# Kernel tuning notes

Hardware: AMD Instinct MI355X
Metric: run time of the kernel (lower is better)

The kernel has to match this reference:

```python
import jax, jax.numpy as jnp
import numpy as np

B, T, I, H, L, O = 32, 2048, 256, 512, 2, 256


def _cell(xg, h, c, Whh, bhh):
    # xg: precomputed/current input-to-hidden projection incl. b_ih, shape [B, 4H]
    gates = xg + h @ Whh.T + bhh
    i, f, g, o = jnp.split(gates, 4, axis=-1)
    i = jax.nn.sigmoid(i)
    f = jax.nn.sigmoid(f)
    g = jnp.tanh(g)
    o = jax.nn.sigmoid(o)
    c2 = f * c + i * g
    h2 = o * jnp.tanh(c2)
    return h2, c2


def setup_inputs() -> dict:
    key = jax.random.key(0)
    ks = jax.random.split(key, 11)
    s_i = 1.0 / np.sqrt(H)
    return {
        "x": jax.random.normal(ks[0], (B, T, I), jnp.float32),
        "W_ih0": jax.random.normal(ks[1], (4 * H, I), jnp.float32) * s_i,
        "W_hh0": jax.random.normal(ks[2], (4 * H, H), jnp.float32) * s_i,
        "b_ih0": jax.random.normal(ks[3], (4 * H,), jnp.float32) * s_i,
        "b_hh0": jax.random.normal(ks[4], (4 * H,), jnp.float32) * s_i,
        "W_ih1": jax.random.normal(ks[5], (4 * H, H), jnp.float32) * s_i,
        "W_hh1": jax.random.normal(ks[6], (4 * H, H), jnp.float32) * s_i,
        "b_ih1": jax.random.normal(ks[7], (4 * H,), jnp.float32) * s_i,
        "b_hh1": jax.random.normal(ks[8], (4 * H,), jnp.float32) * s_i,
        "fc_w": jax.random.normal(ks[9], (O, H), jnp.float32) * s_i,
        "fc_b": jax.random.normal(ks[10], (O,), jnp.float32) * s_i,
    }


def reference(x, W_ih0, W_hh0, b_ih0, b_hh0, W_ih1, W_hh1, b_ih1, b_hh1, fc_w, fc_b):
    # Precompute layer-0 input projections for all timesteps in one big GEMM.
    xproj = jnp.einsum('bti,gi->tbg', x, W_ih0) + b_ih0  # [T, B, 4H]

    h0 = jnp.zeros((x.shape[0], H), x.dtype)
    carry0 = (h0, h0, h0, h0)  # (h_l0, c_l0, h_l1, c_l1)

    def step(carry, xg_t):
        h_0, c_0, h_1, c_1 = carry
        h_0, c_0 = _cell(xg_t, h_0, c_0, W_hh0, b_hh0)
        xg1 = h_0 @ W_ih1.T + b_ih1
        h_1, c_1 = _cell(xg1, h_1, c_1, W_hh1, b_hh1)
        return (h_0, c_0, h_1, c_1), None

    (h_0, c_0, h_1, c_1), _ = jax.lax.scan(step, carry0, xproj)
    # Original takes last timestep's top-layer hidden, then fc.
    return h_1 @ fc_w.T + fc_b
```

## Files before the change

kernel.cpp:

```cpp
#include <hip/hip_runtime.h>
#include <hip/hip_bf16.h>

typedef __hip_bfloat16 bf16;
typedef unsigned long long u64;
typedef unsigned int u32;
typedef unsigned short u16;
using short8 = __attribute__((ext_vector_type(8))) short;
using f32x4  = __attribute__((ext_vector_type(4))) float;

#define T_STEPS 2048
#define IDIM    256
#define HDIM    512
#define NBLK    128
#define R0      8
#define HWW     8192
#define LROW    528
#define TAGMASK 0x0000ffff0000ffffULL

__device__ __forceinline__ float sigm(float x) { return 1.0f / (1.0f + __expf(-x)); }
__device__ __forceinline__ float tanh_f(float x) {
  x = fminf(fmaxf(x, -15.f), 15.f);
  float e = __expf(2.f * x);
  return (e - 1.f) / (e + 1.f);
}
__device__ __forceinline__ u16 bfbits(float f) {
  bf16 b = __float2bfloat16(f); u16 s; __builtin_memcpy(&s, &b, 2); return s;
}
__device__ __forceinline__ short8 cvt8(const float* __restrict__ p) {
  float4 lo = *(const float4*)(const void*)p;
  float4 hi = *(const float4*)(const void*)(p + 4);
  short8 r;
  r[0] = (short)bfbits(lo.x); r[1] = (short)bfbits(lo.y); r[2] = (short)bfbits(lo.z); r[3] = (short)bfbits(lo.w);
  r[4] = (short)bfbits(hi.x); r[5] = (short)bfbits(hi.y); r[6] = (short)bfbits(hi.z); r[7] = (short)bfbits(hi.w);
  return r;
}

__device__ __forceinline__ u64 ldg8(const u64* p) {
  return __hip_atomic_load(p, __ATOMIC_RELAXED, __HIP_MEMORY_SCOPE_AGENT);
}
__device__ __forceinline__ u32 ldg4(const u32* p) {
  return __hip_atomic_load(p, __ATOMIC_RELAXED, __HIP_MEMORY_SCOPE_AGENT);
}
__device__ __forceinline__ void stg4(u32* p, u32 v) {
  __hip_atomic_store(p, v, __ATOMIC_RELAXED, __HIP_MEMORY_SCOPE_AGENT);
}

__device__ __forceinline__ int wave_min_i(int v) {
#pragma unroll
  for (int off = 32; off > 0; off >>= 1) {
    int o = __shfl_xor(v, off, 64);
    v = v < o ? v : o;
  }
  return v;
}

__device__ __forceinline__ void ldsw(bf16* dst, int i, int tid, u64 v) {
  u32 lo = (u32)v, hi = (u32)(v >> 32);
  *(u32*)(void*)(dst + i * LROW + tid * 2) = (lo >> 16) | (hi & 0xffff0000u);
}

__device__ __forceinline__ void pollstage(const u32* __restrict__ src, bf16* dst,
                                          int tid, u32 tag) {
  const u64* s = (const u64*)(const void*)src;
  const u64 tt = ((u64)tag << 32) | tag;
  u64 v[16];
#pragma unroll
  for (int i = 0; i < 16; i++) v[i] = ldg8(s + tid + i * 256);
  unsigned bad = 0xffffu;
  while (bad) {
    unsigned nb = 0;
#pragma unroll
    for (int i = 0; i < 16; i++)
      if (bad & (1u << i)) {
        if ((v[i] & TAGMASK) != tt) { v[i] = ldg8(s + tid + i * 256); nb |= 1u << i; }
      }
    bad = nb;
  }
#pragma unroll
  for (int i = 0; i < 16; i++) ldsw(dst, i, tid, v[i]);
}

__device__ __forceinline__ void poll2stage(const u32* __restrict__ s0p, bf16* d0, u32 tag0,
                                           const u32* __restrict__ s1p, bf16* d1, u32 tag1,
                                           int tid) {
  const u64* s0 = (const u64*)(const void*)s0p;
  const u64* s1 = (const u64*)(const void*)s1p;
  const u64 tt0 = ((u64)tag0 << 32) | tag0;
  const u64 tt1 = ((u64)tag1 << 32) | tag1;
  u64 v0[16], v1[16];
#pragma unroll
  for (int i = 0; i < 16; i++) v0[i] = ldg8(s0 + tid + i * 256);
#pragma unroll
  for (int i = 0; i < 16; i++) v1[i] = ldg8(s1 + tid + i * 256);
  unsigned bad0 = 0xffffu, bad1 = 0xffffu;
  while (bad0 | bad1) {
    unsigned nb0 = 0, nb1 = 0;
#pragma unroll
    for (int i = 0; i < 16; i++)
      if (bad0 & (1u << i)) {
        if ((v0[i] & TAGMASK) != tt0) { v0[i] = ldg8(s0 + tid + i * 256); nb0 |= 1u << i; }
      }
#pragma unroll
    for (int i = 0; i < 16; i++)
      if (bad1 & (1u << i)) {
        if ((v1[i] & TAGMASK) != tt1) { v1[i] = ldg8(s1 + tid + i * 256); nb1 |= 1u << i; }
      }
    bad0 = nb0; bad1 = nb1;
  }
#pragma unroll
  for (int i = 0; i < 16; i++) ldsw(d0, i, tid, v0[i]);
#pragma unroll
  for (int i = 0; i < 16; i++) ldsw(d1, i, tid, v1[i]);
}

#define MFMA(a, b, c) __builtin_amdgcn_mfma_f32_16x16x32_bf16((a), (b), (c), 0, 0, 0)

__global__ void __launch_bounds__(256, 1) lstm_tagged2p(
    const float* __restrict__ x,
    const float* __restrict__ Wih0, const float* __restrict__ Whh0,
    const float* __restrict__ bih0, const float* __restrict__ bhh0,
    const float* __restrict__ Wih1, const float* __restrict__ Whh1,
    const float* __restrict__ bih1, const float* __restrict__ bhh1,
    const float* __restrict__ fcw, const float* __restrict__ fcb,
    float* __restrict__ out,
    u32* __restrict__ ring0g,
    u32* __restrict__ ring1g) {
  __shared__ __align__(16) bf16 lds_h0[16 * LROW];
  __shared__ __align__(16) bf16 lds_h1[16 * LROW];

  const int tid  = threadIdx.x;
  const int w    = tid >> 6, lane = tid & 63;
  const int q    = lane >> 4, m = lane & 15, q8 = q * 8;
  const int bx   = (int)blockIdx.x;
  const int g    = bx >> 6;
  const int rr   = bx & 63;
  const bool l0  = (rr < 32);
  const int blk  = rr & 31;
  const int jb   = blk * 16 + w * 4;
  const int unit = jb + (m >> 2), gate = m & 3;
  const int wrow = gate * HDIM + unit;
  const int ju   = jb + q;
  const f32x4 zero = {0.f, 0.f, 0.f, 0.f};

  u32* ring0 = ring0g + (size_t)g * R0 * HWW;
  u32* ring1 = ring1g + (size_t)g * 2 * HWW;

  short8 A[32];
  f32x4 bias;
  if (l0) {
#pragma unroll
    for (int kc = 0; kc < 8; kc++)  A[kc]      = cvt8(Wih0 + wrow * IDIM + kc * 32 + q8);
#pragma unroll
    for (int kc = 0; kc < 16; kc++) A[8 + kc]  = cvt8(Whh0 + wrow * HDIM + kc * 32 + q8);
#pragma unroll
    for (int r = 0; r < 4; r++)
      bias[r] = bih0[r * HDIM + ju] + bhh0[r * HDIM + ju];
  } else {
#pragma unroll
    for (int kc = 0; kc < 16; kc++) A[kc]      = cvt8(Wih1 + wrow * HDIM + kc * 32 + q8);
#pragma unroll
    for (int kc = 0; kc < 16; kc++) A[16 + kc] = cvt8(Whh1 + wrow * HDIM + kc * 32 + q8);
#pragma unroll
    for (int r = 0; r < 4; r++)
      bias[r] = bih1[r * HDIM + ju] + bhh1[r * HDIM + ju];
  }

  float c_a = 0.f;

  if (l0) {
    f32x4 an0 = bias;
    {
      const float* xa = x + (size_t)(g * 16 + m) * (T_STEPS * IDIM) + q8;
#pragma unroll
      for (int kc = 0; kc < 8; kc++) an0 = MFMA(A[kc], cvt8(xa + kc * 32), an0);
    }
    int est = R0 - 1;
    for (int p = 0; p < T_STEPS; ++p) {
      f32x4 a0 = an0;
      if (p > 0) {
        pollstage(ring0 + ((p - 1) & (R0 - 1)) * HWW, lds_h0, tid, (u32)p);
        __syncthreads();
        f32x4 b0 = zero;
#pragma unroll
        for (int kc = 0; kc < 8; kc++) {
          short8 r0 = *(const short8*)(const void*)(lds_h0 + m * LROW + kc * 32 + q8);
          a0 = MFMA(A[8 + kc], r0, a0);
          short8 s0 = *(const short8*)(const void*)(lds_h0 + m * LROW + (kc + 8) * 32 + q8);
          b0 = MFMA(A[16 + kc], s0, b0);
        }
        a0 = a0 + b0;
      }
      float ia = sigm(a0[0]), fa = sigm(a0[1]), ga = tanh_f(a0[2]), oa = sigm(a0[3]);
      c_a = fa * c_a + ia * ga;
      u32 word = ((u32)bfbits(oa * tanh_f(c_a)) << 16) | (u32)(p + 1);

      if (p >= R0 && est < p) {
        int mn;
        do {
          u32 sw = ldg4(ring1 + (p & 1) * HWW + (lane & 31) * 16);
          mn = wave_min_i((int)(short)(sw & 0xffffu));
        } while (mn < p - (R0 - 1));
        est = mn + (R0 - 1);
      }
      stg4(ring0 + (p & (R0 - 1)) * HWW + (m << 9) + ju, word);

      if (p + 1 < T_STEPS) {
        an0 = bias;
        const float* xa = x + (size_t)(g * 16 + m) * (T_STEPS * IDIM)
                        + (size_t)(p + 1) * IDIM + q8;
#pragma unroll
        for (int kc = 0; kc < 8; kc++) an0 = MFMA(A[kc], cvt8(xa + kc * 32), an0);
      }
      __syncthreads();
    }

    if (blk < 16) {
      pollstage(ring1 + ((T_STEPS - 1) & 1) * HWW, lds_h0, tid, (u32)T_STEPS);
      __syncthreads();
      if (w == 0) {
        const int obase = blk * 16;
        f32x4 a0;
#pragma unroll
        for (int r = 0; r < 4; r++) a0[r] = fcb[obase + 4 * q + r];
        const float* Ar = fcw + (size_t)(obase + m) * HDIM + q8;
#pragma unroll
        for (int kc = 0; kc < 16; kc++) {
          short8 af = cvt8(Ar + kc * 32);
          short8 b0 = *(const short8*)(const void*)(lds_h0 + m * LROW + kc * 32 + q8);
          a0 = MFMA(af, b0, a0);
        }
#pragma unroll
        for (int r = 0; r < 4; r++)
          out[(size_t)(g * 16 + m) * 256 + obase + 4 * q + r] = a0[r];
      }
    }
  } else {
    for (int p = 0; p < T_STEPS; ++p) {
      if (p == 0) {
        pollstage(ring0 + 0 * HWW, lds_h0, tid, 1u);
      } else {
        poll2stage(ring0 + (p & (R0 - 1)) * HWW, lds_h0, (u32)(p + 1),
                   ring1 + ((p - 1) & 1) * HWW,  lds_h1, (u32)p, tid);
      }
      __syncthreads();

      f32x4 c0 = bias, c1 = zero, c2 = zero, c3 = zero;
#pragma unroll
      for (int kc = 0; kc < 8; kc++) {
        short8 r0 = *(const short8*)(const void*)(lds_h0 + m * LROW + kc * 32 + q8);
        c0 = MFMA(A[kc], r0, c0);
        short8 s0 = *(const short8*)(const void*)(lds_h0 + m * LROW + (kc + 8) * 32 + q8);
        c1 = MFMA(A[8 + kc], s0, c1);
      }
      if (p > 0) {
#pragma unroll
        for (int kc = 0; kc < 8; kc++) {
          short8 r0 = *(const short8*)(const void*)(lds_h1 + m * LROW + kc * 32 + q8);
          c2 = MFMA(A[16 + kc], r0, c2);
          short8 s0 = *(const short8*)(const void*)(lds_h1 + m * LROW + (kc + 8) * 32 + q8);
          c3 = MFMA(A[24 + kc], s0, c3);
        }
      }
      f32x4 a0 = (c0 + c1) + (c2 + c3);
      float ia = sigm(a0[0]), fa = sigm(a0[1]), ga = tanh_f(a0[2]), oa = sigm(a0[3]);
      c_a = fa * c_a + ia * ga;
      u32 word = ((u32)bfbits(oa * tanh_f(c_a)) << 16) | (u32)(p + 1);
      stg4(ring1 + (p & 1) * HWW + (m << 9) + ju, word);
      __syncthreads();
    }
  }
}

extern "C" void kernel_launch(void* const* d_in, const int* in_sizes, int n_in,
                              void* d_out, int out_size, void* d_ws, size_t ws_size,
                              hipStream_t stream) {
  const float* x    = (const float*)d_in[0];
  const float* Wih0 = (const float*)d_in[1];
  const float* Whh0 = (const float*)d_in[2];
  const float* bih0 = (const float*)d_in[3];
  const float* bhh0 = (const float*)d_in[4];
  const float* Wih1 = (const float*)d_in[5];
  const float* Whh1 = (const float*)d_in[6];
  const float* bih1 = (const float*)d_in[7];
  const float* bhh1 = (const float*)d_in[8];
  const float* fcw  = (const float*)d_in[9];
  const float* fcb  = (const float*)d_in[10];

  u32* ring0g = (u32*)d_ws;
  u32* ring1g = (u32*)((char*)d_ws + (size_t)2 * R0 * HWW * sizeof(u32));

  hipLaunchKernelGGL(lstm_tagged2p, dim3(NBLK), dim3(256), 0, stream,
                     x, Wih0, Whh0, bih0, bhh0, Wih1, Whh1, bih1, bhh1, fcw, fcb,
                     (float*)d_out, ring0g, ring1g);
}
```

Before: 9.715 ms.

## Probe a sample of ring tags before gathering and split layer-1 waits

Adds a light probe_wait that spins on a small sample of ring tags per wave before the full tagged gather. The goal is to cut the heavy 16-load retry polling traffic on the inter-block rings. In the layer-1 blocks, the combined two-ring poll is split so the layer-0 contribution can be gathered and multiplied before waiting on the layer-1 recurrent state, and the trailing per-step barrier is dropped except at step 0. This lets the two waits overlap with MFMA work, but adds an extra barrier and a second round of probe latency per step.

```diff
diff --git a/kernel.cpp b/kernel.cpp
--- a/kernel.cpp
+++ b/kernel.cpp
@@ -54,13 +54,22 @@
   return v;
 }
 
+__device__ __forceinline__ void probe_wait(const u32* __restrict__ slot, u32 tag, int lane) {
+  const u32* p0 = slot + lane * 8;
+  for (;;) {
+    u32 a = ldg4(p0);
+    u32 b = ldg4(p0 + 4);
+    if (__all(((a & 0xffffu) == tag) && ((b & 0xffffu) == tag))) return;
+  }
+}
+
 __device__ __forceinline__ void ldsw(bf16* dst, int i, int tid, u64 v) {
   u32 lo = (u32)v, hi = (u32)(v >> 32);
   *(u32*)(void*)(dst + i * LROW + tid * 2) = (lo >> 16) | (hi & 0xffff0000u);
 }
 
-__device__ __forceinline__ void pollstage(const u32* __restrict__ src, bf16* dst,
-                                          int tid, u32 tag) {
+__device__ __forceinline__ void gather(const u32* __restrict__ src, bf16* dst,
+                                       int tid, u32 tag) {
   const u64* s = (const u64*)(const void*)src;
   const u64 tt = ((u64)tag << 32) | tag;
   u64 v[16];
@@ -80,42 +89,9 @@
   for (int i = 0; i < 16; i++) ldsw(dst, i, tid, v[i]);
 }
 
-__device__ __forceinline__ void poll2stage(const u32* __restrict__ s0p, bf16* d0, u32 tag0,
-                                           const u32* __restrict__ s1p, bf16* d1, u32 tag1,
-                                           int tid) {
-  const u64* s0 = (const u64*)(const void*)s0p;
-  const u64* s1 = (const u64*)(const void*)s1p;
-  const u64 tt0 = ((u64)tag0 << 32) | tag0;
-  const u64 tt1 = ((u64)tag1 << 32) | tag1;
-  u64 v0[16], v1[16];
-#pragma unroll
-  for (int i = 0; i < 16; i++) v0[i] = ldg8(s0 + tid + i * 256);
-#pragma unroll
-  for (int i = 0; i < 16; i++) v1[i] = ldg8(s1 + tid + i * 256);
-  unsigned bad0 = 0xffffu, bad1 = 0xffffu;
-  while (bad0 | bad1) {
-    unsigned nb0 = 0, nb1 = 0;
-#pragma unroll
-    for (int i = 0; i < 16; i++)
-      if (bad0 & (1u << i)) {
-        if ((v0[i] & TAGMASK) != tt0) { v0[i] = ldg8(s0 + tid + i * 256); nb0 |= 1u << i; }
-      }
-#pragma unroll
-    for (int i = 0; i < 16; i++)
-      if (bad1 & (1u << i)) {
-        if ((v1[i] & TAGMASK) != tt1) { v1[i] = ldg8(s1 + tid + i * 256); nb1 |= 1u << i; }
-      }
-    bad0 = nb0; bad1 = nb1;
-  }
-#pragma unroll
-  for (int i = 0; i < 16; i++) ldsw(d0, i, tid, v0[i]);
-#pragma unroll
-  for (int i = 0; i < 16; i++) ldsw(d1, i, tid, v1[i]);
-}
-
 #define MFMA(a, b, c) __builtin_amdgcn_mfma_f32_16x16x32_bf16((a), (b), (c), 0, 0, 0)
 
-__global__ void __launch_bounds__(256, 1) lstm_tagged2p(
+__global__ void __launch_bounds__(256, 1) lstm_probe2p(
     const float* __restrict__ x,
     const float* __restrict__ Wih0, const float* __restrict__ Whh0,
     const float* __restrict__ bih0, const float* __restrict__ bhh0,
@@ -178,7 +154,8 @@
     for (int p = 0; p < T_STEPS; ++p) {
       f32x4 a0 = an0;
       if (p > 0) {
-        pollstage(ring0 + ((p - 1) & (R0 - 1)) * HWW, lds_h0, tid, (u32)p);
+        probe_wait(ring0 + ((p - 1) & (R0 - 1)) * HWW, (u32)p, lane);
+        gather(ring0 + ((p - 1) & (R0 - 1)) * HWW, lds_h0, tid, (u32)p);
         __syncthreads();
         f32x4 b0 = zero;
 #pragma unroll
@@ -215,7 +192,8 @@
     }
 
     if (blk < 16) {
-      pollstage(ring1 + ((T_STEPS - 1) & 1) * HWW, lds_h0, tid, (u32)T_STEPS);
+      probe_wait(ring1 + ((T_STEPS - 1) & 1) * HWW, (u32)T_STEPS, lane);
+      gather(ring1 + ((T_STEPS - 1) & 1) * HWW, lds_h0, tid, (u32)T_STEPS);
       __syncthreads();
       if (w == 0) {
         const int obase = blk * 16;
@@ -236,12 +214,8 @@
     }
   } else {
     for (int p = 0; p < T_STEPS; ++p) {
-      if (p == 0) {
-        pollstage(ring0 + 0 * HWW, lds_h0, tid, 1u);
-      } else {
-        poll2stage(ring0 + (p & (R0 - 1)) * HWW, lds_h0, (u32)(p + 1),
-                   ring1 + ((p - 1) & 1) * HWW,  lds_h1, (u32)p, tid);
-      }
+      probe_wait(ring0 + (p & (R0 - 1)) * HWW, (u32)(p + 1), lane);
+      gather(ring0 + (p & (R0 - 1)) * HWW, lds_h0, tid, (u32)(p + 1));
       __syncthreads();
 
       f32x4 c0 = bias, c1 = zero, c2 = zero, c3 = zero;
@@ -253,6 +227,9 @@
         c1 = MFMA(A[8 + kc], s0, c1);
       }
       if (p > 0) {
+        probe_wait(ring1 + ((p - 1) & 1) * HWW, (u32)p, lane);
+        gather(ring1 + ((p - 1) & 1) * HWW, lds_h1, tid, (u32)p);
+        __syncthreads();
 #pragma unroll
         for (int kc = 0; kc < 8; kc++) {
           short8 r0 = *(const short8*)(const void*)(lds_h1 + m * LROW + kc * 32 + q8);
@@ -266,7 +243,7 @@
       c_a = fa * c_a + ia * ga;
       u32 word = ((u32)bfbits(oa * tanh_f(c_a)) << 16) | (u32)(p + 1);
       stg4(ring1 + (p & 1) * HWW + (m << 9) + ju, word);
-      __syncthreads();
+      if (p == 0) __syncthreads();
     }
   }
 }
@@ -289,7 +266,7 @@
   u32* ring0g = (u32*)d_ws;
   u32* ring1g = (u32*)((char*)d_ws + (size_t)2 * R0 * HWW * sizeof(u32));
 
-  hipLaunchKernelGGL(lstm_tagged2p, dim3(NBLK), dim3(256), 0, stream,
+  hipLaunchKernelGGL(lstm_probe2p, dim3(NBLK), dim3(256), 0, stream,
                      x, Wih0, Whh0, bih0, bhh0, Wih1, Whh1, bih1, bhh1, fcw, fcb,
                      (float*)d_out, ring0g, ring1g);
 }
```

Result: faster. 8.855 ms (-8.9%).

## Fuse both LSTM layers into one block with sentinel-flag synchronisation

Applied to the files above, without the earlier changes.

Each block now computes both layer 0 (step t) and layer 1 (step t-1), wavefronted, so 64 blocks replace the separate 128 layer-specific blocks and each step needs a single combined wait. Readiness is detected first through small per-wave sentinel arrays polled with a wave-wide __all, and only then are the tagged ring buffers gathered. The separate back-pressure check on the layer-0 ring is dropped. Each block now holds all four weight matrices in registers, which raises register pressure, and halving the block count may lengthen per-step latency.

```diff
diff --git a/kernel.cpp b/kernel.cpp
--- a/kernel.cpp
+++ b/kernel.cpp
@@ -11,8 +11,7 @@
 #define T_STEPS 2048
 #define IDIM    256
 #define HDIM    512
-#define NBLK    128
-#define R0      8
+#define NBLK    64
 #define HWW     8192
 #define LROW    528
 #define TAGMASK 0x0000ffff0000ffffULL
@@ -45,13 +44,19 @@
   __hip_atomic_store(p, v, __ATOMIC_RELAXED, __HIP_MEMORY_SCOPE_AGENT);
 }
 
-__device__ __forceinline__ int wave_min_i(int v) {
-#pragma unroll
-  for (int off = 32; off > 0; off >>= 1) {
-    int o = __shfl_xor(v, off, 64);
-    v = v < o ? v : o;
-  }
-  return v;
+__device__ __forceinline__ void probe1(const u32* __restrict__ s0, u32 t0, int lane) {
+  for (;;) {
+    u32 a = ldg4(s0 + lane), b = ldg4(s0 + 64 + lane);
+    if (__all(a == t0 && b == t0)) return;
+  }
+}
+__device__ __forceinline__ void probe2(const u32* __restrict__ s0, u32 t0,
+                                       const u32* __restrict__ s1, u32 t1, int lane) {
+  for (;;) {
+    u32 a = ldg4(s0 + lane), b = ldg4(s0 + 64 + lane);
+    u32 c = ldg4(s1 + lane), d = ldg4(s1 + 64 + lane);
+    if (__all(a == t0 && b == t0 && c == t1 && d == t1)) return;
+  }
 }
 
 __device__ __forceinline__ void ldsw(bf16* dst, int i, int tid, u64 v) {
@@ -59,8 +64,8 @@
   *(u32*)(void*)(dst + i * LROW + tid * 2) = (lo >> 16) | (hi & 0xffff0000u);
 }
 
-__device__ __forceinline__ void pollstage(const u32* __restrict__ src, bf16* dst,
-                                          int tid, u32 tag) {
+__device__ __forceinline__ void gather1(const u32* __restrict__ src, bf16* dst,
+                                        int tid, u32 tag) {
   const u64* s = (const u64*)(const void*)src;
   const u64 tt = ((u64)tag << 32) | tag;
   u64 v[16];
@@ -79,10 +84,9 @@
 #pragma unroll
   for (int i = 0; i < 16; i++) ldsw(dst, i, tid, v[i]);
 }
-
-__device__ __forceinline__ void poll2stage(const u32* __restrict__ s0p, bf16* d0, u32 tag0,
-                                           const u32* __restrict__ s1p, bf16* d1, u32 tag1,
-                                           int tid) {
+__device__ __forceinline__ void gather2(const u32* __restrict__ s0p, bf16* d0, u32 tag0,
+                                        const u32* __restrict__ s1p, bf16* d1, u32 tag1,
+                                        int tid) {
   const u64* s0 = (const u64*)(const void*)s0p;
   const u64* s1 = (const u64*)(const void*)s1p;
   const u64 tt0 = ((u64)tag0 << 32) | tag0;
@@ -115,7 +119,7 @@
 
 #define MFMA(a, b, c) __builtin_amdgcn_mfma_f32_16x16x32_bf16((a), (b), (c), 0, 0, 0)
 
-__global__ void __launch_bounds__(256, 1) lstm_tagged2p(
+__global__ void __launch_bounds__(256, 1) lstm_onestop(
     const float* __restrict__ x,
     const float* __restrict__ Wih0, const float* __restrict__ Whh0,
     const float* __restrict__ bih0, const float* __restrict__ bhh0,
@@ -123,6 +127,7 @@
     const float* __restrict__ bih1, const float* __restrict__ bhh1,
     const float* __restrict__ fcw, const float* __restrict__ fcb,
     float* __restrict__ out,
+    u32* __restrict__ sentg,
     u32* __restrict__ ring0g,
     u32* __restrict__ ring1g) {
   __shared__ __align__(16) bf16 lds_h0[16 * LROW];
@@ -132,141 +137,133 @@
   const int w    = tid >> 6, lane = tid & 63;
   const int q    = lane >> 4, m = lane & 15, q8 = q * 8;
   const int bx   = (int)blockIdx.x;
-  const int g    = bx >> 6;
-  const int rr   = bx & 63;
-  const bool l0  = (rr < 32);
-  const int blk  = rr & 31;
-  const int jb   = blk * 16 + w * 4;
+  const int g    = bx >> 5;
+  const int blkp = bx & 31;
+  const int jb   = blkp * 16 + w * 4;
   const int unit = jb + (m >> 2), gate = m & 3;
   const int wrow = gate * HDIM + unit;
   const int ju   = jb + q;
+  const int sidx = blkp * 4 + w;
   const f32x4 zero = {0.f, 0.f, 0.f, 0.f};
 
-  u32* ring0 = ring0g + (size_t)g * R0 * HWW;
-  u32* ring1 = ring1g + (size_t)g * 2 * HWW;
-
-  short8 A[32];
-  f32x4 bias;
-  if (l0) {
-#pragma unroll
-    for (int kc = 0; kc < 8; kc++)  A[kc]      = cvt8(Wih0 + wrow * IDIM + kc * 32 + q8);
-#pragma unroll
-    for (int kc = 0; kc < 16; kc++) A[8 + kc]  = cvt8(Whh0 + wrow * HDIM + kc * 32 + q8);
-#pragma unroll
-    for (int r = 0; r < 4; r++)
-      bias[r] = bih0[r * HDIM + ju] + bhh0[r * HDIM + ju];
-  } else {
-#pragma unroll
-    for (int kc = 0; kc < 16; kc++) A[kc]      = cvt8(Wih1 + wrow * HDIM + kc * 32 + q8);
-#pragma unroll
-    for (int kc = 0; kc < 16; kc++) A[16 + kc] = cvt8(Whh1 + wrow * HDIM + kc * 32 + q8);
-#pragma unroll
-    for (int r = 0; r < 4; r++)
-      bias[r] = bih1[r * HDIM + ju] + bhh1[r * HDIM + ju];
-  }
-
-  float c_a = 0.f;
-
-  if (l0) {
-    f32x4 an0 = bias;
-    {
-      const float* xa = x + (size_t)(g * 16 + m) * (T_STEPS * IDIM) + q8;
-#pragma unroll
-      for (int kc = 0; kc < 8; kc++) an0 = MFMA(A[kc], cvt8(xa + kc * 32), an0);
-    }
-    int est = R0 - 1;
-    for (int p = 0; p < T_STEPS; ++p) {
+  u32* sent0 = sentg + (size_t)g * 1024;
+  u32* sent1 = sent0 + 512;
+  u32* ring0 = ring0g + (size_t)g * 4 * HWW;
+  u32* ring1 = ring1g + (size_t)g * 4 * HWW;
+
+  short8 Ax0[8], Ah0[16], Ax1[16], Ah1[16];
+  f32x4 bias0, bias1;
+#pragma unroll
+  for (int kc = 0; kc < 8; kc++)  Ax0[kc] = cvt8(Wih0 + wrow * IDIM + kc * 32 + q8);
+#pragma unroll
+  for (int kc = 0; kc < 16; kc++) Ah0[kc] = cvt8(Whh0 + wrow * HDIM + kc * 32 + q8);
+#pragma unroll
+  for (int kc = 0; kc < 16; kc++) Ax1[kc] = cvt8(Wih1 + wrow * HDIM + kc * 32 + q8);
+#pragma unroll
+  for (int kc = 0; kc < 16; kc++) Ah1[kc] = cvt8(Whh1 + wrow * HDIM + kc * 32 + q8);
+#pragma unroll
+  for (int r = 0; r < 4; r++) {
+    bias0[r] = bih0[r * HDIM + ju] + bhh0[r * HDIM + ju];
+    bias1[r] = bih1[r * HDIM + ju] + bhh1[r * HDIM + ju];
+  }
+
+  float c0 = 0.f, c1 = 0.f;
+
+  f32x4 an0 = bias0;
+  {
+    const float* xa = x + (size_t)(g * 16 + m) * (T_STEPS * IDIM) + q8;
+#pragma unroll
+    for (int kc = 0; kc < 8; kc++) an0 = MFMA(Ax0[kc], cvt8(xa + kc * 32), an0);
+  }
+
+  for (int t = 0; t <= T_STEPS; ++t) {
+    if (t > 0) {
+      if (t > 1) {
+        probe2(sent0 + ((t - 1) & 3) * 128, (u32)t,
+               sent1 + ((t - 2) & 3) * 128, (u32)(t - 1), lane);
+        gather2(ring0 + ((t - 1) & 3) * HWW, lds_h0, (u32)t,
+                ring1 + ((t - 2) & 3) * HWW, lds_h1, (u32)(t - 1), tid);
+      } else {
+        probe1(sent0 + 0 * 128, 1u, lane);
+        gather1(ring0 + 0 * HWW, lds_h0, tid, 1u);
+      }
+      __syncthreads();
+    }
+
+    if (t < T_STEPS) {
       f32x4 a0 = an0;
-      if (p > 0) {
-        pollstage(ring0 + ((p - 1) & (R0 - 1)) * HWW, lds_h0, tid, (u32)p);
-        __syncthreads();
+      if (t > 0) {
         f32x4 b0 = zero;
 #pragma unroll
         for (int kc = 0; kc < 8; kc++) {
           short8 r0 = *(const short8*)(const void*)(lds_h0 + m * LROW + kc * 32 + q8);
-          a0 = MFMA(A[8 + kc], r0, a0);
+          a0 = MFMA(Ah0[kc], r0, a0);
           short8 s0 = *(const short8*)(const void*)(lds_h0 + m * LROW + (kc + 8) * 32 + q8);
-          b0 = MFMA(A[16 + kc], s0, b0);
+          b0 = MFMA(Ah0[kc + 8], s0, b0);
         }
         a0 = a0 + b0;
       }
       float ia = sigm(a0[0]), fa = sigm(a0[1]), ga = tanh_f(a0[2]), oa = sigm(a0[3]);
-      c_a = fa * c_a + ia * ga;
-      u32 word = ((u32)bfbits(oa * tanh_f(c_a)) << 16) | (u32)(p + 1);
-
-      if (p >= R0 && est < p) {
-        int mn;
-        do {
-          u32 sw = ldg4(ring1 + (p & 1) * HWW + (lane & 31) * 16);
-          mn = wave_min_i((int)(short)(sw & 0xffffu));
-        } while (mn < p - (R0 - 1));
-        est = mn + (R0 - 1);
-      }
-      stg4(ring0 + (p & (R0 - 1)) * HWW + (m << 9) + ju, word);
-
-      if (p + 1 < T_STEPS) {
-        an0 = bias;
-        const float* xa = x + (size_t)(g * 16 + m) * (T_STEPS * IDIM)
-                        + (size_t)(p + 1) * IDIM + q8;
-#pragma unroll
-        for (int kc = 0; kc < 8; kc++) an0 = MFMA(A[kc], cvt8(xa + kc * 32), an0);
-      }
-      __syncthreads();
-    }
-
-    if (blk < 16) {
-      pollstage(ring1 + ((T_STEPS - 1) & 1) * HWW, lds_h0, tid, (u32)T_STEPS);
-      __syncthreads();
-      if (w == 0) {
-        const int obase = blk * 16;
-        f32x4 a0;
-#pragma unroll
-        for (int r = 0; r < 4; r++) a0[r] = fcb[obase + 4 * q + r];
-        const float* Ar = fcw + (size_t)(obase + m) * HDIM + q8;
-#pragma unroll
-        for (int kc = 0; kc < 16; kc++) {
-          short8 af = cvt8(Ar + kc * 32);
-          short8 b0 = *(const short8*)(const void*)(lds_h0 + m * LROW + kc * 32 + q8);
-          a0 = MFMA(af, b0, a0);
-        }
-#pragma unroll
-        for (int r = 0; r < 4; r++)
-          out[(size_t)(g * 16 + m) * 256 + obase + 4 * q + r] = a0[r];
-      }
-    }
-  } else {
-    for (int p = 0; p < T_STEPS; ++p) {
-      if (p == 0) {
-        pollstage(ring0 + 0 * HWW, lds_h0, tid, 1u);
-      } else {
-        poll2stage(ring0 + (p & (R0 - 1)) * HWW, lds_h0, (u32)(p + 1),
-                   ring1 + ((p - 1) & 1) * HWW,  lds_h1, (u32)p, tid);
-      }
-      __syncthreads();
-
-      f32x4 c0 = bias, c1 = zero, c2 = zero, c3 = zero;
+      c0 = fa * c0 + ia * ga;
+      u32 word = ((u32)bfbits(oa * tanh_f(c0)) << 16) | (u32)(t + 1);
+      stg4(ring0 + (t & 3) * HWW + (m << 9) + ju, word);
+      if (lane == 0) stg4(sent0 + (t & 3) * 128 + sidx, (u32)(t + 1));
+    }
+
+    if (t > 0) {
+      f32x4 g0 = bias1, g1 = zero, g2 = zero, g3 = zero;
 #pragma unroll
       for (int kc = 0; kc < 8; kc++) {
         short8 r0 = *(const short8*)(const void*)(lds_h0 + m * LROW + kc * 32 + q8);
-        c0 = MFMA(A[kc], r0, c0);
+        g0 = MFMA(Ax1[kc], r0, g0);
         short8 s0 = *(const short8*)(const void*)(lds_h0 + m * LROW + (kc + 8) * 32 + q8);
-        c1 = MFMA(A[8 + kc], s0, c1);
-      }
-      if (p > 0) {
+        g1 = MFMA(Ax1[kc + 8], s0, g1);
+      }
+      if (t > 1) {
 #pragma unroll
         for (int kc = 0; kc < 8; kc++) {
           short8 r0 = *(const short8*)(const void*)(lds_h1 + m * LROW + kc * 32 + q8);
-          c2 = MFMA(A[16 + kc], r0, c2);
+          g2 = MFMA(Ah1[kc], r0, g2);
           short8 s0 = *(const short8*)(const void*)(lds_h1 + m * LROW + (kc + 8) * 32 + q8);
-          c3 = MFMA(A[24 + kc], s0, c3);
+          g3 = MFMA(Ah1[kc + 8], s0, g3);
         }
       }
-      f32x4 a0 = (c0 + c1) + (c2 + c3);
-      float ia = sigm(a0[0]), fa = sigm(a0[1]), ga = tanh_f(a0[2]), oa = sigm(a0[3]);
-      c_a = fa * c_a + ia * ga;
-      u32 word = ((u32)bfbits(oa * tanh_f(c_a)) << 16) | (u32)(p + 1);
-      stg4(ring1 + (p & 1) * HWW + (m << 9) + ju, word);
-      __syncthreads();
+      f32x4 a1 = (g0 + g1) + (g2 + g3);
+      float ia = sigm(a1[0]), fa = sigm(a1[1]), ga = tanh_f(a1[2]), oa = sigm(a1[3]);
+      c1 = fa * c1 + ia * ga;
+      u32 word = ((u32)bfbits(oa * tanh_f(c1)) << 16) | (u32)t;
+      stg4(ring1 + ((t - 1) & 3) * HWW + (m << 9) + ju, word);
+      if (lane == 0) stg4(sent1 + ((t - 1) & 3) * 128 + sidx, (u32)t);
+    }
+
+    if (t + 1 < T_STEPS) {
+      an0 = bias0;
+      const float* xa = x + (size_t)(g * 16 + m) * (T_STEPS * IDIM)
+                      + (size_t)(t + 1) * IDIM + q8;
+#pragma unroll
+      for (int kc = 0; kc < 8; kc++) an0 = MFMA(Ax0[kc], cvt8(xa + kc * 32), an0);
+    }
+  }
+
+  if (blkp < 16) {
+    probe1(sent1 + ((T_STEPS - 1) & 3) * 128, (u32)T_STEPS, lane);
+    gather1(ring1 + ((T_STEPS - 1) & 3) * HWW, lds_h0, tid, (u32)T_STEPS);
+    __syncthreads();
+    if (w == 0) {
+      const int obase = blkp * 16;
+      f32x4 a0;
+#pragma unroll
+      for (int r = 0; r < 4; r++) a0[r] = fcb[obase + 4 * q + r];
+      const float* Ar = fcw + (size_t)(obase + m) * HDIM + q8;
+#pragma unroll
+      for (int kc = 0; kc < 16; kc++) {
+        short8 af = cvt8(Ar + kc * 32);
+        short8 b0 = *(const short8*)(const void*)(lds_h0 + m * LROW + kc * 32 + q8);
+        a0 = MFMA(af, b0, a0);
+      }
+#pragma unroll
+      for (int r = 0; r < 4; r++)
+        out[(size_t)(g * 16 + m) * 256 + obase + 4 * q + r] = a0[r];
     }
   }
 }
@@ -286,10 +283,11 @@
   const float* fcw  = (const float*)d_in[9];
   const float* fcb  = (const float*)d_in[10];
 
-  u32* ring0g = (u32*)d_ws;
-  u32* ring1g = (u32*)((char*)d_ws + (size_t)2 * R0 * HWW * sizeof(u32));
-
-  hipLaunchKernelGGL(lstm_tagged2p, dim3(NBLK), dim3(256), 0, stream,
+  u32* sentg  = (u32*)d_ws;
+  u32* ring0g = (u32*)((char*)d_ws + 8192);
+  u32* ring1g = (u32*)((char*)d_ws + 8192 + (size_t)2 * 4 * HWW * sizeof(u32));
+
+  hipLaunchKernelGGL(lstm_onestop, dim3(NBLK), dim3(256), 0, stream,
                      x, Wih0, Whh0, bih0, bhh0, Wih1, Whh1, bih1, bhh1, fcw, fcb,
-                     (float*)d_out, ring0g, ring1g);
-}
+                     (float*)d_out, sentg, ring0g, ring1g);
+}
```

Measured after the change: 17.64 ms. 81.5% more time.
